# Kernel tuning notes

Measured on AMD Instinct MI355X. Metric: run time of the kernel, lower is better.

## Reference

```python
import jax, jax.numpy as jnp
import numpy as np

BLANK = 0  # blank_index


def lstm_step(x, h, c, W_ih, W_hh, b_ih, b_hh):
    # torch LSTM gate order: i, f, g, o
    gates = x @ W_ih.T + h @ W_hh.T + b_ih + b_hh  # (B, 4H)
    i, f, g, o = jnp.split(gates, 4, axis=-1)
    c2 = jax.nn.sigmoid(f) * c + jax.nn.sigmoid(i) * jnp.tanh(g)
    h2 = jax.nn.sigmoid(o) * jnp.tanh(c2)
    return h2, c2


def greedy_decode(encoder_output, encoded_lengths, embedding, W_ih, W_hh, b_ih, b_hh,
                  W_enc, b_enc, W_pred, b_pred, W_out, b_out, h0, c0):
    # encoder_output: (B, H, T) -> (B, T, H), as in forward()'s transpose(1, 2)
    x = jnp.transpose(encoder_output, (0, 2, 1))
    B, T, H = x.shape

    def step(carry, inputs):
        h, c, last_label = carry          # h,c: (1,B,H); last_label: (B,) int32
        f_t, t = inputs                   # f_t: (B,H) encoder frame, t: scalar int32
        # _pred_step: SOS (zero vector) at t==0, else embed last emitted label
        emb = jnp.where(t == 0, jnp.zeros((B, H), x.dtype), embedding[last_label])
        h1, c1 = lstm_step(emb, h[0], c[0], W_ih, W_hh, b_ih, b_hh)
        # _joint_step: additive joint + relu + output proj, log_softmax (CPU path)
        joint = jax.nn.relu(f_t @ W_enc.T + b_enc + h1 @ W_pred.T + b_pred)
        logp = jax.nn.log_softmax((joint @ W_out.T + b_out).astype(jnp.float32), axis=-1)
        k = jnp.argmax(logp, axis=-1).astype(jnp.int32)  # (B,)
        # blank if past this utterance's length OR argmax is blank
        blank_mask = (t >= encoded_lengths) | (k == BLANK)
        m = blank_mask[:, None]
        # blank entries keep old RNN state and old last_label (original's gather/scatter)
        h_new = jnp.where(m, h[0], h1)[None]
        c_new = jnp.where(m, c[0], c1)[None]
        new_label = jnp.where(blank_mask, last_label, k)
        emitted = jnp.where(blank_mask, BLANK, k)  # blank == nothing emitted this step
        return (h_new, c_new, new_label), emitted

    init = (h0, c0, jnp.full((B,), BLANK, jnp.int32))
    xs = (jnp.transpose(x, (1, 0, 2)), jnp.arange(T, dtype=jnp.int32))
    (hF, cF, _), emitted = jax.lax.scan(step, init, xs)  # emitted: (T, B)
    return emitted.T, hF, cF  # labels (B,T) blank-padded, final (h, c)


def setup_inputs() -> dict:
    key = jax.random.key(0)
    ks = jax.random.split(key, 15)
    B, T, H, V1 = 128, 512, 640, 4097
    s = jnp.float32(0.1)
    return {
        "encoder_output": jax.random.normal(ks[0], (B, H, T), jnp.float32),
        "encoded_lengths": jax.random.randint(ks[1], (B,), 0, T).astype(jnp.int32),
        "embedding": jax.random.normal(ks[2], (V1, H), jnp.float32) * s,
        "W_ih": jax.random.normal(ks[3], (4 * H, H), jnp.float32) * s,
        "W_hh": jax.random.normal(ks[4], (4 * H, H), jnp.float32) * s,
        "b_ih": jax.random.normal(ks[5], (4 * H,), jnp.float32) * s,
        "b_hh": jax.random.normal(ks[6], (4 * H,), jnp.float32) * s,
        "W_enc": jax.random.normal(ks[7], (H, H), jnp.float32) * s,
        "b_enc": jax.random.normal(ks[8], (H,), jnp.float32) * s,
        "W_pred": jax.random.normal(ks[9], (H, H), jnp.float32) * s,
        "b_pred": jax.random.normal(ks[10], (H,), jnp.float32) * s,
        "W_out": jax.random.normal(ks[11], (V1, H), jnp.float32) * s,
        "b_out": jax.random.normal(ks[12], (V1,), jnp.float32) * s,
        "h0": jnp.zeros((1, B, H), jnp.float32),
        "c0": jnp.zeros((1, B, H), jnp.float32),
    }


def reference(encoder_output, encoded_lengths, embedding, W_ih, W_hh, b_ih, b_hh,
              W_enc, b_enc, W_pred, b_pred, W_out, b_out, h0, c0):
    return greedy_decode(encoder_output, encoded_lengths, embedding, W_ih, W_hh,
                         b_ih, b_hh, W_enc, b_enc, W_pred, b_pred, W_out, b_out, h0, c0)
```

## Files before the change

kernel.cpp:

```cpp
#include <hip/hip_runtime.h>
#include <stdint.h>

#define HH 640
#define BB 128
#define TT 512
#define VV 4097
#define G4 2560
#define VP3 4104
#define VE  4112

typedef float f32x4v __attribute__((ext_vector_type(4)));

__device__ __forceinline__ float sigm(float x){ return 1.0f/(1.0f+expf(-x)); }

__device__ __forceinline__ unsigned long long packkey(float f, unsigned v){
    unsigned u = __float_as_uint(f);
    unsigned m = (u & 0x80000000u) ? ~u : (u | 0x80000000u);
    return ((unsigned long long)m << 32) | (unsigned long long)(~v);
}
__device__ __forceinline__ int xcd_tile(int bid, int per){ return (bid & 7)*per + (bid >> 3); }
__device__ __forceinline__ size_t taddr(int k, int b){
    return ((size_t)(k>>2)*BB + b)*4 + (k&3);
}

__global__ __launch_bounds__(256) void k_init3(const float* __restrict__ h0, const float* __restrict__ c0,
                       float* __restrict__ hs0, float* __restrict__ csT,
                       int* __restrict__ label, unsigned long long* __restrict__ slot8){
    int i = blockIdx.x*256 + threadIdx.x;
    if (i < BB*HH){
        int b = i / HH, jj = i % HH;
        size_t o = taddr(jj, b);
        hs0[o] = h0[i]; csT[o] = c0[i];
    }
    if (i < BB) label[i] = 0;
    if (i < 8*BB) slot8[i] = 0ULL;
}

__global__ __launch_bounds__(256) void k_tr_gate(const float* __restrict__ W, float* __restrict__ WT){
    int idx = blockIdx.x*256 + threadIdx.x;
    if (idx >= G4*160) return;
    int row = idx / 160, kq = idx % 160;
    int g = row / HH, jj = row % HH;
    float4 f = *reinterpret_cast<const float4*>(W + (size_t)row*HH + kq*4);
    WT[(size_t)(kq*4+0)*G4 + jj*4+g] = f.x;
    WT[(size_t)(kq*4+1)*G4 + jj*4+g] = f.y;
    WT[(size_t)(kq*4+2)*G4 + jj*4+g] = f.z;
    WT[(size_t)(kq*4+3)*G4 + jj*4+g] = f.w;
}
__global__ __launch_bounds__(256) void k_tr640(const float* __restrict__ W, float* __restrict__ WT){
    int idx = blockIdx.x*256 + threadIdx.x;
    if (idx >= HH*160) return;
    int n = idx / 160, kq = idx % 160;
    float4 f = *reinterpret_cast<const float4*>(W + (size_t)n*HH + kq*4);
    WT[(size_t)(kq*4+0)*HH + n] = f.x;
    WT[(size_t)(kq*4+1)*HH + n] = f.y;
    WT[(size_t)(kq*4+2)*HH + n] = f.z;
    WT[(size_t)(kq*4+3)*HH + n] = f.w;
}
__global__ __launch_bounds__(256) void k_tr_wout3(const float* __restrict__ W, float* __restrict__ WT){
    int idx = blockIdx.x*256 + threadIdx.x;
    if (idx >= VP3*160) return;
    int v = idx / 160, kq = idx % 160;
    float4 f = make_float4(0.f,0.f,0.f,0.f);
    if (v < VV) f = *reinterpret_cast<const float4*>(W + (size_t)v*HH + kq*4);
    WT[(size_t)(kq*4+0)*VP3 + v] = f.x;
    WT[(size_t)(kq*4+1)*VP3 + v] = f.y;
    WT[(size_t)(kq*4+2)*VP3 + v] = f.z;
    WT[(size_t)(kq*4+3)*VP3 + v] = f.w;
}
__global__ __launch_bounds__(256) void k_boutpad3(const float* __restrict__ b_out, float* __restrict__ boutP){
    int v = blockIdx.x*256 + threadIdx.x;
    if (v < VP3) boutP[v] = (v < VV) ? b_out[v] : -1e30f;
}
__global__ __launch_bounds__(256) void k_tr_embT(const float* __restrict__ emb, float* __restrict__ embT){
    int idx = blockIdx.x*256 + threadIdx.x;
    if (idx >= 160*VE) return;
    int kq = idx / VE, v = idx % VE;
    float4 f = make_float4(0.f,0.f,0.f,0.f);
    if (v < VV) f = *reinterpret_cast<const float4*>(emb + (size_t)v*HH + kq*4);
    embT[(size_t)(kq*4+0)*VE + v] = f.x;
    embT[(size_t)(kq*4+1)*VE + v] = f.y;
    embT[(size_t)(kq*4+2)*VE + v] = f.z;
    embT[(size_t)(kq*4+3)*VE + v] = f.w;
}

__global__ __launch_bounds__(256) void k_embproj3(const float* __restrict__ embT,
                          const float* __restrict__ WihT,
                          const float* __restrict__ b_ih, const float* __restrict__ b_hh,
                          float* __restrict__ embproj){
    __shared__ float lwv[HH*16];
    int vt = blockIdx.x / 160, ut = blockIdx.x % 160;
    for (int i=threadIdx.x; i<HH*16; i+=256)
        lwv[i] = WihT[(size_t)(i>>4)*G4 + ut*16 + (i&15)];
    float bias[16];
    #pragma unroll
    for (int u=0;u<16;++u){
        int gu = ut*16+u, jj = gu>>2, g = gu&3;
        bias[u] = b_ih[g*HH+jj] + b_hh[g*HH+jj];
    }
    __syncthreads();
    int v = vt*256 + threadIdx.x;
    float acc[16];
    #pragma unroll
    for (int u=0;u<16;++u) acc[u]=0.f;
    if (v < VV){
        #pragma unroll 2
        for (int k=0;k<HH;++k){
            float e = embT[(size_t)k*VE + v];
            const f32x4v* wr = reinterpret_cast<const f32x4v*>(&lwv[k*16]);
            #pragma unroll
            for (int g=0; g<4; ++g){
                f32x4v w = wr[g];
                #pragma unroll
                for (int ee=0; ee<4; ++ee) acc[g*4+ee] = fmaf(w[ee], e, acc[g*4+ee]);
            }
        }
    }
    if (v <= VV){
        #pragma unroll
        for (int q=0;q<4;++q){
            float4 st = make_float4(acc[q*4+0]+bias[q*4+0], acc[q*4+1]+bias[q*4+1],
                                    acc[q*4+2]+bias[q*4+2], acc[q*4+3]+bias[q*4+3]);
            *reinterpret_cast<float4*>(embproj + (size_t)v*G4 + ut*16 + q*4) = st;
        }
    }
}

__global__ __launch_bounds__(128) void k_encprojT2(const float* __restrict__ x,
                          const float* __restrict__ WencT, const float* __restrict__ b_enc,
                          float* __restrict__ encprojT){
    int tile = (blockIdx.x & 7)*2560 + (blockIdx.x >> 3);
    int b   = tile / 160;
    int rem = tile % 160;
    int tt  = rem / 5;
    int nt2 = rem % 5;
    int n = nt2*128 + threadIdx.x;
    float acc[16];
    #pragma unroll
    for (int i=0;i<16;i++) acc[i]=0.f;
    const float* xb = x + (size_t)b*HH*TT + tt*16;
    #pragma unroll 4
    for (int k=0;k<HH;++k){
        float wv = WencT[(size_t)k*HH + n];
        const float4* xp = reinterpret_cast<const float4*>(xb + (size_t)k*TT);
        float4 x0=xp[0], x1=xp[1], x2=xp[2], x3=xp[3];
        acc[0]=fmaf(x0.x,wv,acc[0]);  acc[1]=fmaf(x0.y,wv,acc[1]);
        acc[2]=fmaf(x0.z,wv,acc[2]);  acc[3]=fmaf(x0.w,wv,acc[3]);
        acc[4]=fmaf(x1.x,wv,acc[4]);  acc[5]=fmaf(x1.y,wv,acc[5]);
        acc[6]=fmaf(x1.z,wv,acc[6]);  acc[7]=fmaf(x1.w,wv,acc[7]);
        acc[8]=fmaf(x2.x,wv,acc[8]);  acc[9]=fmaf(x2.y,wv,acc[9]);
        acc[10]=fmaf(x2.z,wv,acc[10]); acc[11]=fmaf(x2.w,wv,acc[11]);
        acc[12]=fmaf(x3.x,wv,acc[12]); acc[13]=fmaf(x3.y,wv,acc[13]);
        acc[14]=fmaf(x3.z,wv,acc[14]); acc[15]=fmaf(x3.w,wv,acc[15]);
    }
    float be = b_enc[n];
    #pragma unroll
    for (int ti=0; ti<16; ++ti)
        encprojT[((size_t)(tt*16+ti)*HH + n)*BB + b] = acc[ti] + be;
}


__global__ __launch_bounds__(512) void kA(
    const float* __restrict__ WhhT, const float* __restrict__ embproj,
    const int* __restrict__ lens,
    const float* __restrict__ hsrT, float* __restrict__ hswT,
    const float* __restrict__ h1rT, float* __restrict__ h1wT,
    float* __restrict__ csT, float* __restrict__ c1T,
    int* __restrict__ label, const unsigned long long* __restrict__ slot8,
    float* __restrict__ out_emit, int t)
{
    __shared__ float lw[HH*16];
    __shared__ float red[3*16*128];
    const int bid = xcd_tile(blockIdx.x, 20);
    const int tid = threadIdx.x;
    const int b = tid & 127, kh = tid >> 7;
    const int u0 = bid*16;

    for (int i=tid; i<HH*16; i+=512)
        lw[i] = WhhT[(size_t)(i>>4)*G4 + u0 + (i&15)];

    bool mask; int sel=0, kprev=0;
    if (t==0){ mask=true; sel=0; }
    else{
        unsigned long long key = slot8[b];
        #pragma unroll
        for (int q=1;q<8;++q){ unsigned long long o=slot8[q*128+b]; if(o>key)key=o; }
        int k = (int)(~(unsigned)key);
        int lab = label[b];
        mask = ((t-1) >= lens[b]) || (k==0);
        kprev = k; sel = mask ? lab : k;
    }
    __syncthreads();

    const float4* hp = reinterpret_cast<const float4*>(mask ? hsrT : h1rT);
    float a1[16];
    #pragma unroll
    for (int u=0;u<16;++u) a1[u]=0.f;
    const int k0 = kh*40;
    #pragma unroll 2
    for (int k4=k0; k4<k0+40; ++k4){
        float4 hv = hp[(size_t)k4*BB + b];
        #pragma unroll
        for (int q=0;q<4;++q){
            float h = (q==0)?hv.x:(q==1)?hv.y:(q==2)?hv.z:hv.w;
            const f32x4v* wr = reinterpret_cast<const f32x4v*>(&lw[(k4*4+q)*16]);
            #pragma unroll
            for (int g=0; g<4; ++g){
                f32x4v w = wr[g];
                #pragma unroll
                for (int ee=0; ee<4; ++ee) a1[g*4+ee] = fmaf(w[ee], h, a1[g*4+ee]);
            }
        }
    }
    if (kh > 0){
        #pragma unroll
        for (int u=0;u<16;++u) red[((kh-1)*16+u)*128 + b] = a1[u];
    }
    __syncthreads();
    if (kh == 0){
        int erow = (t==0) ? VV : sel;
        const float4* eb = reinterpret_cast<const float4*>(embproj + (size_t)erow*G4 + u0);
        const size_t g4 = (size_t)bid*BB + b;
        float4 ce4 = mask ? reinterpret_cast<const float4*>(csT)[g4]
                          : reinterpret_cast<const float4*>(c1T)[g4];
        float4 he4 = mask ? reinterpret_cast<const float4*>(hsrT)[g4]
                          : reinterpret_cast<const float4*>(h1rT)[g4];
        float cn[4], hn[4];
        const float* cep = &ce4.x;
        #pragma unroll
        for (int jl=0; jl<4; ++jl){
            float4 e = eb[jl];
            float gi = a1[jl*4+0] + red[(jl*4+0)*128+b] + red[(16+jl*4+0)*128+b] + red[(32+jl*4+0)*128+b] + e.x;
            float gf = a1[jl*4+1] + red[(jl*4+1)*128+b] + red[(16+jl*4+1)*128+b] + red[(32+jl*4+1)*128+b] + e.y;
            float gg = a1[jl*4+2] + red[(jl*4+2)*128+b] + red[(16+jl*4+2)*128+b] + red[(32+jl*4+2)*128+b] + e.z;
            float go = a1[jl*4+3] + red[(jl*4+3)*128+b] + red[(16+jl*4+3)*128+b] + red[(32+jl*4+3)*128+b] + e.w;
            float ce = cep[jl];
            float cv = sigm(gf)*ce + sigm(gi)*tanhf(gg);
            cn[jl] = cv;
            hn[jl] = sigm(go)*tanhf(cv);
        }
        reinterpret_cast<float4*>(csT)[g4]  = ce4;
        reinterpret_cast<float4*>(c1T)[g4]  = make_float4(cn[0],cn[1],cn[2],cn[3]);
        reinterpret_cast<float4*>(hswT)[g4] = he4;
        reinterpret_cast<float4*>(h1wT)[g4] = make_float4(hn[0],hn[1],hn[2],hn[3]);
        if (bid == 0){
            if (t > 0) out_emit[(size_t)b*TT + (t-1)] = mask ? 0.f : (float)kprev;
            label[b] = sel;
        }
    }
}

__global__ __launch_bounds__(512) void kB(
    const float* __restrict__ WpredT, const float* __restrict__ encprojT,
    const float* __restrict__ b_pred, const float* __restrict__ h1T,
    float* __restrict__ jointT, unsigned long long* __restrict__ slot8, int t)
{
    __shared__ float lw[HH*4];
    __shared__ float red[3*4*128];
    const int bid = xcd_tile(blockIdx.x, 20);
    const int tid = threadIdx.x;
    const int b = tid & 127, kh = tid >> 7;
    const int n0 = bid*4;
    for (int i=tid; i<HH*4; i+=512)
        lw[i] = WpredT[(size_t)(i>>2)*HH + n0 + (i&3)];
    if (bid == 0 && kh == 3){
        #pragma unroll
        for (int q=0;q<8;++q) slot8[q*128 + b] = 0ULL;
    }
    __syncthreads();
    const float4* hp = reinterpret_cast<const float4*>(h1T);
    float a[4] = {0.f,0.f,0.f,0.f};
    const int k0 = kh*40;
    #pragma unroll 2
    for (int k4=k0; k4<k0+40; ++k4){
        float4 hv = hp[(size_t)k4*BB + b];
        #pragma unroll
        for (int q=0;q<4;++q){
            float h = (q==0)?hv.x:(q==1)?hv.y:(q==2)?hv.z:hv.w;
            f32x4v w = *reinterpret_cast<const f32x4v*>(&lw[(k4*4+q)*4]);
            #pragma unroll
            for (int ee=0; ee<4; ++ee) a[ee] = fmaf(w[ee], h, a[ee]);
        }
    }
    if (kh > 0){
        #pragma unroll
        for (int u=0;u<4;++u) red[((kh-1)*4+u)*128 + b] = a[u];
    }
    __syncthreads();
    if (kh == 0){
        float jn[4];
        #pragma unroll
        for (int u=0;u<4;++u){
            float s = a[u] + red[u*128+b] + red[(4+u)*128+b] + red[(8+u)*128+b]
                    + b_pred[n0+u] + encprojT[((size_t)t*HH + n0+u)*BB + b];
            jn[u] = fmaxf(s, 0.f);
        }
        reinterpret_cast<float4*>(jointT)[(size_t)bid*BB + b] =
            make_float4(jn[0],jn[1],jn[2],jn[3]);
    }
}

__global__ __launch_bounds__(512) void kC(
    const float* __restrict__ WoutT3, const float* __restrict__ boutP3,
    const float* __restrict__ jointT, unsigned long long* __restrict__ slot8)
{
    __shared__ float lw[HH*20];
    __shared__ float red[3*19*128];
    const int bid = xcd_tile(blockIdx.x, 27);
    const int tid = threadIdx.x;
    const int b = tid & 127, kh = tid >> 7;
    const int v0 = bid*19;
    for (int i=tid; i<HH*19; i+=512){
        int k = i/19, u = i - k*19;
        lw[k*20 + u] = WoutT3[(size_t)k*VP3 + v0 + u];
    }
    __syncthreads();
    const float4* jp = reinterpret_cast<const float4*>(jointT);
    float a[19];
    #pragma unroll
    for (int u=0;u<19;++u) a[u]=0.f;
    const int k0 = kh*40;
    #pragma unroll 2
    for (int k4=k0; k4<k0+40; ++k4){
        float4 jv = jp[(size_t)k4*BB + b];
        #pragma unroll
        for (int q=0;q<4;++q){
            float h = (q==0)?jv.x:(q==1)?jv.y:(q==2)?jv.z:jv.w;
            const f32x4v* wr = reinterpret_cast<const f32x4v*>(&lw[(k4*4+q)*20]);
            #pragma unroll
            for (int g=0; g<4; ++g){
                f32x4v w = wr[g];
                #pragma unroll
                for (int ee=0; ee<4; ++ee) a[g*4+ee] = fmaf(w[ee], h, a[g*4+ee]);
            }
            f32x4v w4 = wr[4];
            a[16] = fmaf(w4[0], h, a[16]);
            a[17] = fmaf(w4[1], h, a[17]);
            a[18] = fmaf(w4[2], h, a[18]);
        }
    }
    if (kh > 0){
        #pragma unroll
        for (int u=0;u<19;++u) red[((kh-1)*19+u)*128 + b] = a[u];
    }
    __syncthreads();
    if (kh == 0){
        unsigned long long key = 0ULL;
        #pragma unroll
        for (int u=0;u<19;++u){
            float s = a[u] + red[u*128+b] + red[(19+u)*128+b] + red[(38+u)*128+b] + boutP3[v0+u];
            unsigned long long kk = packkey(s, (unsigned)(v0+u));
            if (kk > key) key = kk;
        }
        atomicMax(&slot8[(bid&7)*128 + b], key);
    }
}

__global__ __launch_bounds__(256) void kFin(const int* __restrict__ lens,
                        const unsigned long long* __restrict__ slot8,
                        const float* __restrict__ hsT, const float* __restrict__ h1T,
                        const float* __restrict__ csT, const float* __restrict__ c1T,
                        float* __restrict__ dout)
{
    int i = blockIdx.x*256 + threadIdx.x;
    if (i >= BB*HH) return;
    int b = i / HH, jj = i % HH;
    unsigned long long key = slot8[b];
    #pragma unroll
    for (int q=1;q<8;++q){ unsigned long long o=slot8[q*128+b]; if(o>key)key=o; }
    int k = (int)(~(unsigned)key);
    bool m = ((TT-1) >= lens[b]) || (k == 0);
    size_t o = taddr(jj, b);
    dout[BB*TT + i]         = m ? hsT[o] : h1T[o];
    dout[BB*TT + BB*HH + i] = m ? csT[o] : c1T[o];
    if (i < BB){
        unsigned long long key2 = slot8[i];
        #pragma unroll
        for (int q=1;q<8;++q){ unsigned long long o2=slot8[q*128+i]; if(o2>key2)key2=o2; }
        int k2 = (int)(~(unsigned)key2);
        bool mm = ((TT-1) >= lens[i]) || (k2 == 0);
        dout[(size_t)i*TT + (TT-1)] = mm ? 0.0f : (float)k2;
    }
}

__global__ __launch_bounds__(256) void k_init(const float* __restrict__ h0, const float* __restrict__ c0,
                       float* __restrict__ hs0, float* __restrict__ cs,
                       int* __restrict__ label, unsigned long long* __restrict__ slot){
    int i = blockIdx.x*256 + threadIdx.x;
    if (i < BB*HH){ hs0[i] = h0[i]; cs[i] = c0[i]; }
    if (i < BB){ label[i] = 0; slot[i] = 0ULL; }
}

__global__ __launch_bounds__(256) void k_p1o(
    const float* __restrict__ Whh, const float* __restrict__ Wih,
    const float* __restrict__ embedding,
    const float* __restrict__ b_ih, const float* __restrict__ b_hh,
    const int* __restrict__ lens,
    const float* __restrict__ hs_r, float* __restrict__ hs_w,
    const float* __restrict__ h1_r, float* __restrict__ h1_w,
    float* c_state, float* c1, int* label,
    const unsigned long long* __restrict__ slot,
    float* __restrict__ out_emit, int t)
{
    int tile = (blockIdx.x & 7)*20 + (blockIdx.x >> 3);
    int jt = tile >> 4, bg = tile & 15;
    int lane = threadIdx.x & 63, w = threadIdx.x >> 6;
    int j = (jt<<6) + lane, b0 = bg<<3;

    bool mask[8]; int kprev[8]; int sel[8];
    #pragma unroll
    for (int bi=0; bi<8; ++bi){
        int b = b0+bi;
        if (t == 0){ mask[bi]=true; sel[bi]=0; kprev[bi]=0; }
        else {
            unsigned long long key = slot[b];
            int k = (int)(~(unsigned)key);
            int lab = label[b];
            bool m = ((t-1) >= lens[b]) || (k == 0);
            mask[bi]=m; kprev[bi]=k; sel[bi] = m ? lab : k;
        }
    }
    float acc[8];
    #pragma unroll
    for (int i=0;i<8;i++) acc[i]=0.f;
    const float* wrow  = Whh + (size_t)(w*HH + j)*HH;
    const float* wrow2 = Wih + (size_t)(w*HH + j)*HH;
    for (int kc=0; kc<HH; kc+=16){
        float wv[16], wv2[16];
        #pragma unroll
        for (int q=0;q<4;q++){
            float4 f = *reinterpret_cast<const float4*>(wrow + kc + q*4);
            wv[q*4+0]=f.x; wv[q*4+1]=f.y; wv[q*4+2]=f.z; wv[q*4+3]=f.w;
            float4 f2 = *reinterpret_cast<const float4*>(wrow2 + kc + q*4);
            wv2[q*4+0]=f2.x; wv2[q*4+1]=f2.y; wv2[q*4+2]=f2.z; wv2[q*4+3]=f2.w;
        }
        #pragma unroll
        for (int bi=0; bi<8; ++bi){
            int b = b0+bi;
            const float* hp0 = hs_r + (size_t)b*HH + kc;
            const float* hp1 = h1_r + (size_t)b*HH + kc;
            float a = acc[bi];
            if (mask[bi]){
                #pragma unroll
                for (int k=0;k<16;k++) a = fmaf(hp0[k], wv[k], a);
            } else {
                #pragma unroll
                for (int k=0;k<16;k++) a = fmaf(hp1[k], wv[k], a);
            }
            if (t > 0){
                const float* ep = embedding + (size_t)sel[bi]*HH + kc;
                #pragma unroll
                for (int k=0;k<16;k++) a = fmaf(ep[k], wv2[k], a);
            }
            acc[bi] = a;
        }
    }
    __shared__ float xch[8][4][64];
    #pragma unroll
    for (int bi=0; bi<8; ++bi)
        xch[bi][w][lane] = acc[bi] + b_ih[w*HH + j] + b_hh[w*HH + j];
    __syncthreads();
    #pragma unroll
    for (int r=0; r<2; ++r){
        int bi = (w<<1) + r;
        int b  = b0 + bi;
        size_t o = (size_t)b*HH + j;
        float gi = xch[bi][0][lane], gf = xch[bi][1][lane];
        float gg = xch[bi][2][lane], go = xch[bi][3][lane];
        float ce = mask[bi] ? c_state[o] : c1[o];
        float c2 = sigm(gf)*ce + sigm(gi)*tanhf(gg);
        float h2 = sigm(go)*tanhf(c2);
        float he = mask[bi] ? hs_r[o] : h1_r[o];
        c_state[o] = ce; c1[o] = c2; hs_w[o] = he; h1_w[o] = h2;
    }
    if (jt == 0 && t > 0 && threadIdx.x < 8){
        int bi = threadIdx.x; int b = b0 + bi;
        out_emit[(size_t)b*TT + (t-1)] = mask[bi] ? 0.0f : (float)kprev[bi];
        label[b] = sel[bi];
    }
}

__global__ __launch_bounds__(128) void k_p2o(
    const float* __restrict__ Wpred, const float* __restrict__ Wenc,
    const float* __restrict__ x, const float* __restrict__ b_enc,
    const float* __restrict__ b_pred, const float* __restrict__ h1,
    float* __restrict__ joint, unsigned long long* __restrict__ slot, int t)
{
    int tile = (blockIdx.x & 7)*20 + (blockIdx.x >> 3);
    int nt = tile / 32, bg = tile % 32;
    int lane = threadIdx.x & 63, w = threadIdx.x >> 6;
    int n = nt*128 + w*64 + lane, b0 = bg*4;
    float acc[4] = {0.f,0.f,0.f,0.f};
    const float* wr  = Wpred + (size_t)n*HH;
    const float* wr2 = Wenc  + (size_t)n*HH;
    for (int kc=0; kc<HH; kc+=16){
        float wv[16], wv2[16];
        #pragma unroll
        for (int q=0;q<4;q++){
            float4 f = *reinterpret_cast<const float4*>(wr + kc + q*4);
            wv[q*4+0]=f.x; wv[q*4+1]=f.y; wv[q*4+2]=f.z; wv[q*4+3]=f.w;
            float4 f2 = *reinterpret_cast<const float4*>(wr2 + kc + q*4);
            wv2[q*4+0]=f2.x; wv2[q*4+1]=f2.y; wv2[q*4+2]=f2.z; wv2[q*4+3]=f2.w;
        }
        #pragma unroll
        for (int bi=0; bi<4; ++bi){
            int b = b0+bi;
            const float* hp = h1 + (size_t)b*HH + kc;
            float a = acc[bi];
            #pragma unroll
            for (int k=0;k<16;k++) a = fmaf(hp[k], wv[k], a);
            const float* xp = x + (size_t)b*HH*TT + (size_t)kc*TT + t;
            #pragma unroll
            for (int k=0;k<16;k++) a = fmaf(xp[(size_t)k*TT], wv2[k], a);
            acc[bi] = a;
        }
    }
    #pragma unroll
    for (int bi=0; bi<4; ++bi){
        int b = b0+bi;
        joint[(size_t)b*HH + n] = fmaxf(acc[bi] + b_pred[n] + b_enc[n], 0.0f);
    }
    if (tile == 0) slot[threadIdx.x] = 0ULL;
}

__global__ __launch_bounds__(256) void k_p3o(
    const float* __restrict__ Wout, const float* __restrict__ b_out,
    const float* __restrict__ joint, unsigned long long* __restrict__ slot)
{
    int tile = (blockIdx.x & 7)*34 + (blockIdx.x >> 3);
    int vt = tile >> 4, bg = tile & 15;
    int lane = threadIdx.x & 63, w = threadIdx.x >> 6;
    int v = vt*256 + w*64 + lane;
    bool valid = v < VV;
    int vv = valid ? v : (VV-1);
    int b0 = bg*8;
    float acc[8];
    #pragma unroll
    for (int i=0;i<8;i++) acc[i]=0.f;
    const float* wr = Wout + (size_t)vv*HH;
    for (int kc=0; kc<HH; kc+=16){
        float wv[16];
        #pragma unroll
        for (int q=0;q<4;q++){
            float4 f = *reinterpret_cast<const float4*>(wr + kc + q*4);
            wv[q*4+0]=f.x; wv[q*4+1]=f.y; wv[q*4+2]=f.z; wv[q*4+3]=f.w;
        }
        #pragma unroll
        for (int bi=0; bi<8; ++bi){
            int b = b0+bi;
            const float* jp = joint + (size_t)b*HH + kc;
            float a = acc[bi];
            #pragma unroll
            for (int k=0;k<16;k++) a = fmaf(jp[k], wv[k], a);
            acc[bi] = a;
        }
    }
    float bofl = b_out[vv];
    __shared__ unsigned long long redo[4][8];
    #pragma unroll
    for (int bi=0; bi<8; ++bi){
        unsigned long long key = valid ? packkey(acc[bi] + bofl, (unsigned)v) : 0ULL;
        #pragma unroll
        for (int off=32; off>0; off>>=1){
            unsigned long long o = __shfl_xor(key, off, 64);
            if (o > key) key = o;
        }
        if (lane == 0) redo[w][bi] = key;
    }
    __syncthreads();
    if (threadIdx.x < 8){
        int bi = threadIdx.x;
        unsigned long long m = redo[0][bi];
        #pragma unroll
        for (int q=1;q<4;q++) if (redo[q][bi] > m) m = redo[q][bi];
        atomicMax(&slot[b0+bi], m);
    }
}

__global__ __launch_bounds__(256) void k_finalo(const int* __restrict__ lens,
                        const unsigned long long* __restrict__ slot,
                        const float* __restrict__ hs_r, const float* __restrict__ h1_r,
                        const float* __restrict__ cs,  const float* __restrict__ c1,
                        float* __restrict__ dout)
{
    int i = blockIdx.x*256 + threadIdx.x;
    if (i >= BB*HH) return;
    int b = i / HH;
    unsigned long long key = slot[b];
    int k = (int)(~(unsigned)key);
    bool m = ((TT-1) >= lens[b]) || (k == 0);
    dout[BB*TT + i]         = m ? hs_r[i] : h1_r[i];
    dout[BB*TT + BB*HH + i] = m ? cs[i]   : c1[i];
    if (i < BB){
        unsigned long long key2 = slot[i];
        int k2 = (int)(~(unsigned)key2);
        bool mm = ((TT-1) >= lens[i]) || (k2 == 0);
        dout[(size_t)i*TT + (TT-1)] = mm ? 0.0f : (float)k2;
    }
}

extern "C" void kernel_launch(void* const* d_in, const int* in_sizes, int n_in,
                              void* d_out, int out_size, void* d_ws, size_t ws_size,
                              hipStream_t stream)
{
    const float* x     = (const float*)d_in[0];
    const int*   lens  = (const int*)  d_in[1];
    const float* emb   = (const float*)d_in[2];
    const float* Wih   = (const float*)d_in[3];
    const float* Whh   = (const float*)d_in[4];
    const float* bih   = (const float*)d_in[5];
    const float* bhh   = (const float*)d_in[6];
    const float* Wenc  = (const float*)d_in[7];
    const float* benc  = (const float*)d_in[8];
    const float* Wpred = (const float*)d_in[9];
    const float* bpred = (const float*)d_in[10];
    const float* Wout  = (const float*)d_in[11];
    const float* bout  = (const float*)d_in[12];
    const float* h0    = (const float*)d_in[13];
    const float* c0    = (const float*)d_in[14];
    float* out = (float*)d_out;
    (void)in_sizes; (void)n_in; (void)out_size;

    char* ws = (char*)d_ws;
    size_t off = 0;
    auto alloc = [&](size_t bytes) -> void* {
        void* p = ws + off; off += (bytes + 255) & ~(size_t)255; return p;
    };
    auto aligned = [](size_t bytes){ return (bytes + 255) & ~(size_t)255; };

    const size_t BH = (size_t)BB*HH*sizeof(float);
    float* hs0  = (float*)alloc(BH);
    float* hs1  = (float*)alloc(BH);
    float* h1b0 = (float*)alloc(BH);
    float* h1b1 = (float*)alloc(BH);
    float* cs   = (float*)alloc(BH);
    float* c1   = (float*)alloc(BH);
    float* joint= (float*)alloc(BH);
    int* label  = (int*)alloc(BB*sizeof(int));
    unsigned long long* slot8 = (unsigned long long*)alloc(8*BB*sizeof(unsigned long long));

    size_t need = off
        + aligned((size_t)HH*G4*sizeof(float))
        + aligned((size_t)HH*G4*sizeof(float))
        + aligned((size_t)HH*HH*sizeof(float))
        + aligned((size_t)HH*HH*sizeof(float))
        + aligned((size_t)HH*VP3*sizeof(float))
        + aligned((size_t)VP3*sizeof(float))
        + aligned((size_t)HH*VE*sizeof(float))
        + aligned((size_t)(VV+1)*G4*sizeof(float))
        + aligned((size_t)TT*BB*HH*sizeof(float));

    if (ws_size >= need){
        float* WhhT   = (float*)alloc((size_t)HH*G4*sizeof(float));
        float* WihT   = (float*)alloc((size_t)HH*G4*sizeof(float));
        float* WpredT = (float*)alloc((size_t)HH*HH*sizeof(float));
        float* WencT  = (float*)alloc((size_t)HH*HH*sizeof(float));
        float* WoutT3 = (float*)alloc((size_t)HH*VP3*sizeof(float));
        float* boutP3 = (float*)alloc((size_t)VP3*sizeof(float));
        float* embT   = (float*)alloc((size_t)HH*VE*sizeof(float));
        float* embproj= (float*)alloc((size_t)(VV+1)*G4*sizeof(float));
        float* encprojT=(float*)alloc((size_t)TT*BB*HH*sizeof(float));

        k_init3<<<(BB*HH+255)/256, 256, 0, stream>>>(h0, c0, hs0, cs, label, slot8);
        k_tr_gate<<<(G4*160+255)/256, 256, 0, stream>>>(Whh, WhhT);
        k_tr_gate<<<(G4*160+255)/256, 256, 0, stream>>>(Wih, WihT);
        k_tr640 <<<(HH*160+255)/256, 256, 0, stream>>>(Wpred, WpredT);
        k_tr640 <<<(HH*160+255)/256, 256, 0, stream>>>(Wenc,  WencT);
        k_tr_wout3<<<(VP3*160+255)/256, 256, 0, stream>>>(Wout, WoutT3);
        k_boutpad3<<<(VP3+255)/256, 256, 0, stream>>>(bout, boutP3);
        k_tr_embT<<<(160*VE+255)/256, 256, 0, stream>>>(emb, embT);
        k_embproj3<<<17*160, 256, 0, stream>>>(embT, WihT, bih, bhh, embproj);
        k_encprojT2<<<20480, 128, 0, stream>>>(x, WencT, benc, encprojT);

        float* hsbuf[2] = {hs0, hs1};
        float* h1buf[2] = {h1b0, h1b1};
        for (int t = 0; t < TT; ++t){
            const float* hsr = hsbuf[t & 1];
            float*       hsw = hsbuf[(t+1) & 1];
            const float* h1r = h1buf[(t+1) & 1];
            float*       h1w = h1buf[t & 1];
            kA<<<160, 512, 0, stream>>>(WhhT, embproj, lens, hsr, hsw, h1r, h1w,
                                        cs, c1, label, slot8, out, t);
            kB<<<160, 512, 0, stream>>>(WpredT, encprojT, bpred, h1w, joint, slot8, t);
            kC<<<216, 512, 0, stream>>>(WoutT3, boutP3, joint, slot8);
        }
        kFin<<<(BB*HH+255)/256, 256, 0, stream>>>(lens, slot8, hsbuf[0], h1buf[1], cs, c1, out);
        return;
    }

    unsigned long long* slot = slot8;
    k_init<<<(BB*HH+255)/256, 256, 0, stream>>>(h0, c0, hs0, cs, label, slot);
    float* hsbuf[2] = {hs0, hs1};
    float* h1buf[2] = {h1b0, h1b1};
    for (int t = 0; t < TT; ++t){
        const float* hsr = hsbuf[t & 1];
        float*       hsw = hsbuf[(t+1) & 1];
        const float* h1r = h1buf[(t+1) & 1];
        float*       h1w = h1buf[t & 1];
        k_p1o<<<160, 256, 0, stream>>>(Whh, Wih, emb, bih, bhh, lens,
                                       hsr, hsw, h1r, h1w, cs, c1, label, slot, out, t);
        k_p2o<<<160, 128, 0, stream>>>(Wpred, Wenc, x, benc, bpred, h1w, joint, slot, t);
        k_p3o<<<272, 256, 0, stream>>>(Wout, bout, joint, slot);
    }
    k_finalo<<<(BB*HH+255)/256, 256, 0, stream>>>(lens, slot, hsbuf[0], h1buf[1], cs, c1, out);
}
```

Measured before the change: 33.09 ms.

## Pre-pack per-block weight tiles contiguously and rebalance output projection to 16-wide tiles

```diff
diff --git a/kernel.cpp b/kernel.cpp
--- a/kernel.cpp
+++ b/kernel.cpp
@@ -6,8 +6,7 @@
 #define TT 512
 #define VV 4097
 #define G4 2560
-#define VP3 4104
-#define VE  4112
+#define VP3 4352
 
 typedef float f32x4v __attribute__((ext_vector_type(4)));
 
@@ -57,7 +56,7 @@
     WT[(size_t)(kq*4+2)*HH + n] = f.z;
     WT[(size_t)(kq*4+3)*HH + n] = f.w;
 }
-__global__ __launch_bounds__(256) void k_tr_wout3(const float* __restrict__ W, float* __restrict__ WT){
+__global__ __launch_bounds__(256) void k_tr_woutr(const float* __restrict__ W, float* __restrict__ WT){
     int idx = blockIdx.x*256 + threadIdx.x;
     if (idx >= VP3*160) return;
     int v = idx / 160, kq = idx % 160;
@@ -68,30 +67,43 @@
     WT[(size_t)(kq*4+2)*VP3 + v] = f.z;
     WT[(size_t)(kq*4+3)*VP3 + v] = f.w;
 }
-__global__ __launch_bounds__(256) void k_boutpad3(const float* __restrict__ b_out, float* __restrict__ boutP){
+__global__ __launch_bounds__(256) void k_boutp(const float* __restrict__ b_out, float* __restrict__ bp){
     int v = blockIdx.x*256 + threadIdx.x;
-    if (v < VP3) boutP[v] = (v < VV) ? b_out[v] : -1e30f;
-}
-__global__ __launch_bounds__(256) void k_tr_embT(const float* __restrict__ emb, float* __restrict__ embT){
-    int idx = blockIdx.x*256 + threadIdx.x;
-    if (idx >= 160*VE) return;
-    int kq = idx / VE, v = idx % VE;
-    float4 f = make_float4(0.f,0.f,0.f,0.f);
-    if (v < VV) f = *reinterpret_cast<const float4*>(emb + (size_t)v*HH + kq*4);
-    embT[(size_t)(kq*4+0)*VE + v] = f.x;
-    embT[(size_t)(kq*4+1)*VE + v] = f.y;
-    embT[(size_t)(kq*4+2)*VE + v] = f.z;
-    embT[(size_t)(kq*4+3)*VE + v] = f.w;
-}
-
-__global__ __launch_bounds__(256) void k_embproj3(const float* __restrict__ embT,
+    if (v < VP3) bp[v] = (v < VV) ? b_out[v] : -1e30f;
+}
+
+__global__ __launch_bounds__(256) void k_packA(const float* __restrict__ WhhT, float* __restrict__ WhhP){
+    int i = blockIdx.x*256 + threadIdx.x;
+    if (i >= 160*HH*4) return;
+    int bid = i / (HH*4), rem = i % (HH*4);
+    int k = rem >> 2, q = rem & 3;
+    reinterpret_cast<float4*>(WhhP)[i] =
+        *reinterpret_cast<const float4*>(&WhhT[(size_t)k*G4 + bid*16 + q*4]);
+}
+__global__ __launch_bounds__(256) void k_packB(const float* __restrict__ WpredT, float* __restrict__ WpredP){
+    int i = blockIdx.x*256 + threadIdx.x;
+    if (i >= 160*HH) return;
+    int bid = i / HH, k = i % HH;
+    reinterpret_cast<float4*>(WpredP)[i] =
+        *reinterpret_cast<const float4*>(&WpredT[(size_t)k*HH + bid*4]);
+}
+__global__ __launch_bounds__(256) void k_packC(const float* __restrict__ WoutTr, float* __restrict__ WoutP){
+    int i = blockIdx.x*256 + threadIdx.x;
+    if (i >= 272*HH*4) return;
+    int bid = i / (HH*4), rem = i % (HH*4);
+    int k = rem >> 2, q = rem & 3;
+    reinterpret_cast<float4*>(WoutP)[i] =
+        *reinterpret_cast<const float4*>(&WoutTr[(size_t)k*VP3 + bid*16 + q*4]);
+}
+
+__global__ __launch_bounds__(256) void k_embproj2(const float* __restrict__ emb,
                           const float* __restrict__ WihT,
                           const float* __restrict__ b_ih, const float* __restrict__ b_hh,
                           float* __restrict__ embproj){
-    __shared__ float lwv[HH*16];
+    __shared__ float lw[640*16];
     int vt = blockIdx.x / 160, ut = blockIdx.x % 160;
-    for (int i=threadIdx.x; i<HH*16; i+=256)
-        lwv[i] = WihT[(size_t)(i>>4)*G4 + ut*16 + (i&15)];
+    for (int i=threadIdx.x; i<640*16; i+=256)
+        lw[i] = WihT[(size_t)(i>>4)*G4 + ut*16 + (i&15)];
     float bias[16];
     #pragma unroll
     for (int u=0;u<16;++u){
@@ -104,15 +116,19 @@
     #pragma unroll
     for (int u=0;u<16;++u) acc[u]=0.f;
     if (v < VV){
-        #pragma unroll 2
-        for (int k=0;k<HH;++k){
-            float e = embT[(size_t)k*VE + v];
-            const f32x4v* wr = reinterpret_cast<const f32x4v*>(&lwv[k*16]);
+        const float4* er = reinterpret_cast<const float4*>(emb + (size_t)v*HH);
+        for (int k4=0;k4<160;++k4){
+            float4 ev = er[k4];
             #pragma unroll
-            for (int g=0; g<4; ++g){
-                f32x4v w = wr[g];
+            for (int q=0;q<4;++q){
+                float e = (q==0)?ev.x:(q==1)?ev.y:(q==2)?ev.z:ev.w;
+                const f32x4v* wr = reinterpret_cast<const f32x4v*>(&lw[(k4*4+q)*16]);
                 #pragma unroll
-                for (int ee=0; ee<4; ++ee) acc[g*4+ee] = fmaf(w[ee], e, acc[g*4+ee]);
+                for (int g=0; g<4; ++g){
+                    f32x4v w = wr[g];
+                    #pragma unroll
+                    for (int ee=0; ee<4; ++ee) acc[g*4+ee] = fmaf(w[ee], e, acc[g*4+ee]);
+                }
             }
         }
     }
@@ -161,7 +177,7 @@
 
 
 __global__ __launch_bounds__(512) void kA(
-    const float* __restrict__ WhhT, const float* __restrict__ embproj,
+    const float* __restrict__ WhhP, const float* __restrict__ embproj,
     const int* __restrict__ lens,
     const float* __restrict__ hsrT, float* __restrict__ hswT,
     const float* __restrict__ h1rT, float* __restrict__ h1wT,
@@ -176,8 +192,11 @@
     const int b = tid & 127, kh = tid >> 7;
     const int u0 = bid*16;
 
-    for (int i=tid; i<HH*16; i+=512)
-        lw[i] = WhhT[(size_t)(i>>4)*G4 + u0 + (i&15)];
+    {
+        const float4* wsrc = reinterpret_cast<const float4*>(WhhP + (size_t)bid*(HH*16));
+        float4* ld = reinterpret_cast<float4*>(lw);
+        for (int i=tid; i<HH*4; i+=512) ld[i] = wsrc[i];
+    }
 
     bool mask; int sel=0, kprev=0;
     if (t==0){ mask=true; sel=0; }
@@ -197,7 +216,7 @@
     #pragma unroll
     for (int u=0;u<16;++u) a1[u]=0.f;
     const int k0 = kh*40;
-    #pragma unroll 2
+    #pragma unroll 4
     for (int k4=k0; k4<k0+40; ++k4){
         float4 hv = hp[(size_t)k4*BB + b];
         #pragma unroll
@@ -251,7 +270,7 @@
 }
 
 __global__ __launch_bounds__(512) void kB(
-    const float* __restrict__ WpredT, const float* __restrict__ encprojT,
+    const float* __restrict__ WpredP, const float* __restrict__ encprojT,
     const float* __restrict__ b_pred, const float* __restrict__ h1T,
     float* __restrict__ jointT, unsigned long long* __restrict__ slot8, int t)
 {
@@ -261,8 +280,11 @@
     const int tid = threadIdx.x;
     const int b = tid & 127, kh = tid >> 7;
     const int n0 = bid*4;
-    for (int i=tid; i<HH*4; i+=512)
-        lw[i] = WpredT[(size_t)(i>>2)*HH + n0 + (i&3)];
+    {
+        const float4* wsrc = reinterpret_cast<const float4*>(WpredP + (size_t)bid*(HH*4));
+        float4* ld = reinterpret_cast<float4*>(lw);
+        for (int i=tid; i<HH; i+=512) ld[i] = wsrc[i];
+    }
     if (bid == 0 && kh == 3){
         #pragma unroll
         for (int q=0;q<8;++q) slot8[q*128 + b] = 0ULL;
@@ -271,7 +293,7 @@
     const float4* hp = reinterpret_cast<const float4*>(h1T);
     float a[4] = {0.f,0.f,0.f,0.f};
     const int k0 = kh*40;
-    #pragma unroll 2
+    #pragma unroll 4
     for (int k4=k0; k4<k0+40; ++k4){
         float4 hv = hp[(size_t)k4*BB + b];
         #pragma unroll
@@ -301,54 +323,51 @@
 }
 
 __global__ __launch_bounds__(512) void kC(
-    const float* __restrict__ WoutT3, const float* __restrict__ boutP3,
+    const float* __restrict__ WoutP, const float* __restrict__ boutP,
     const float* __restrict__ jointT, unsigned long long* __restrict__ slot8)
 {
-    __shared__ float lw[HH*20];
-    __shared__ float red[3*19*128];
-    const int bid = xcd_tile(blockIdx.x, 27);
+    __shared__ float lw[HH*16];
+    __shared__ float red[3*16*128];
+    const int bid = xcd_tile(blockIdx.x, 34);
     const int tid = threadIdx.x;
     const int b = tid & 127, kh = tid >> 7;
-    const int v0 = bid*19;
-    for (int i=tid; i<HH*19; i+=512){
-        int k = i/19, u = i - k*19;
-        lw[k*20 + u] = WoutT3[(size_t)k*VP3 + v0 + u];
+    const int v0 = bid*16;
+    {
+        const float4* wsrc = reinterpret_cast<const float4*>(WoutP + (size_t)bid*(HH*16));
+        float4* ld = reinterpret_cast<float4*>(lw);
+        for (int i=tid; i<HH*4; i+=512) ld[i] = wsrc[i];
     }
     __syncthreads();
     const float4* jp = reinterpret_cast<const float4*>(jointT);
-    float a[19];
-    #pragma unroll
-    for (int u=0;u<19;++u) a[u]=0.f;
+    float a[16];
+    #pragma unroll
+    for (int u=0;u<16;++u) a[u]=0.f;
     const int k0 = kh*40;
-    #pragma unroll 2
+    #pragma unroll 4
     for (int k4=k0; k4<k0+40; ++k4){
         float4 jv = jp[(size_t)k4*BB + b];
         #pragma unroll
         for (int q=0;q<4;++q){
             float h = (q==0)?jv.x:(q==1)?jv.y:(q==2)?jv.z:jv.w;
-            const f32x4v* wr = reinterpret_cast<const f32x4v*>(&lw[(k4*4+q)*20]);
+            const f32x4v* wr = reinterpret_cast<const f32x4v*>(&lw[(k4*4+q)*16]);
             #pragma unroll
             for (int g=0; g<4; ++g){
                 f32x4v w = wr[g];
                 #pragma unroll
                 for (int ee=0; ee<4; ++ee) a[g*4+ee] = fmaf(w[ee], h, a[g*4+ee]);
             }
-            f32x4v w4 = wr[4];
-            a[16] = fmaf(w4[0], h, a[16]);
-            a[17] = fmaf(w4[1], h, a[17]);
-            a[18] = fmaf(w4[2], h, a[18]);
         }
     }
     if (kh > 0){
         #pragma unroll
-        for (int u=0;u<19;++u) red[((kh-1)*19+u)*128 + b] = a[u];
+        for (int u=0;u<16;++u) red[((kh-1)*16+u)*128 + b] = a[u];
     }
     __syncthreads();
     if (kh == 0){
         unsigned long long key = 0ULL;
         #pragma unroll
-        for (int u=0;u<19;++u){
-            float s = a[u] + red[u*128+b] + red[(19+u)*128+b] + red[(38+u)*128+b] + boutP3[v0+u];
+        for (int u=0;u<16;++u){
+            float s = a[u] + red[u*128+b] + red[(16+u)*128+b] + red[(32+u)*128+b] + boutP[v0+u];
             unsigned long long kk = packkey(s, (unsigned)(v0+u));
             if (kk > key) key = kk;
         }
@@ -384,10 +403,10 @@
 }
 
 __global__ __launch_bounds__(256) void k_init(const float* __restrict__ h0, const float* __restrict__ c0,
-                       float* __restrict__ hs0, float* __restrict__ cs,
+                       float* __restrict__ hs0, float* __restrict__ cso,
                        int* __restrict__ label, unsigned long long* __restrict__ slot){
     int i = blockIdx.x*256 + threadIdx.x;
-    if (i < BB*HH){ hs0[i] = h0[i]; cs[i] = c0[i]; }
+    if (i < BB*HH){ hs0[i] = h0[i]; cso[i] = c0[i]; }
     if (i < BB){ label[i] = 0; slot[i] = 0ULL; }
 }
 
@@ -398,7 +417,7 @@
     const int* __restrict__ lens,
     const float* __restrict__ hs_r, float* __restrict__ hs_w,
     const float* __restrict__ h1_r, float* __restrict__ h1_w,
-    float* c_state, float* c1, int* label,
+    float* c_state, float* c1o, int* label,
     const unsigned long long* __restrict__ slot,
     float* __restrict__ out_emit, int t)
 {
@@ -461,17 +480,17 @@
         xch[bi][w][lane] = acc[bi] + b_ih[w*HH + j] + b_hh[w*HH + j];
     __syncthreads();
     #pragma unroll
-    for (int r=0; r<2; ++r){
-        int bi = (w<<1) + r;
+    for (int rr=0; rr<2; ++rr){
+        int bi = (w<<1) + rr;
         int b  = b0 + bi;
         size_t o = (size_t)b*HH + j;
         float gi = xch[bi][0][lane], gf = xch[bi][1][lane];
         float gg = xch[bi][2][lane], go = xch[bi][3][lane];
-        float ce = mask[bi] ? c_state[o] : c1[o];
+        float ce = mask[bi] ? c_state[o] : c1o[o];
         float c2 = sigm(gf)*ce + sigm(gi)*tanhf(gg);
         float h2 = sigm(go)*tanhf(c2);
         float he = mask[bi] ? hs_r[o] : h1_r[o];
-        c_state[o] = ce; c1[o] = c2; hs_w[o] = he; h1_w[o] = h2;
+        c_state[o] = ce; c1o[o] = c2; hs_w[o] = he; h1_w[o] = h2;
     }
     if (jt == 0 && t > 0 && threadIdx.x < 8){
         int bi = threadIdx.x; int b = b0 + bi;
@@ -580,7 +599,7 @@
 __global__ __launch_bounds__(256) void k_finalo(const int* __restrict__ lens,
                         const unsigned long long* __restrict__ slot,
                         const float* __restrict__ hs_r, const float* __restrict__ h1_r,
-                        const float* __restrict__ cs,  const float* __restrict__ c1,
+                        const float* __restrict__ cso,  const float* __restrict__ c1o,
                         float* __restrict__ dout)
 {
     int i = blockIdx.x*256 + threadIdx.x;
@@ -590,7 +609,7 @@
     int k = (int)(~(unsigned)key);
     bool m = ((TT-1) >= lens[b]) || (k == 0);
     dout[BB*TT + i]         = m ? hs_r[i] : h1_r[i];
-    dout[BB*TT + BB*HH + i] = m ? cs[i]   : c1[i];
+    dout[BB*TT + BB*HH + i] = m ? cso[i]  : c1o[i];
     if (i < BB){
         unsigned long long key2 = slot[i];
         int k2 = (int)(~(unsigned)key2);
@@ -626,8 +645,6 @@
     auto alloc = [&](size_t bytes) -> void* {
         void* p = ws + off; off += (bytes + 255) & ~(size_t)255; return p;
     };
-    auto aligned = [](size_t bytes){ return (bytes + 255) & ~(size_t)255; };
-
     const size_t BH = (size_t)BB*HH*sizeof(float);
     float* hs0  = (float*)alloc(BH);
     float* hs1  = (float*)alloc(BH);
@@ -638,38 +655,33 @@
     float* joint= (float*)alloc(BH);
     int* label  = (int*)alloc(BB*sizeof(int));
     unsigned long long* slot8 = (unsigned long long*)alloc(8*BB*sizeof(unsigned long long));
-
-    size_t need = off
-        + aligned((size_t)HH*G4*sizeof(float))
-        + aligned((size_t)HH*G4*sizeof(float))
-        + aligned((size_t)HH*HH*sizeof(float))
-        + aligned((size_t)HH*HH*sizeof(float))
-        + aligned((size_t)HH*VP3*sizeof(float))
-        + aligned((size_t)VP3*sizeof(float))
-        + aligned((size_t)HH*VE*sizeof(float))
-        + aligned((size_t)(VV+1)*G4*sizeof(float))
-        + aligned((size_t)TT*BB*HH*sizeof(float));
+    float* boutP = (float*)alloc((size_t)VP3*sizeof(float));
+    float* WencT = (float*)alloc((size_t)HH*HH*sizeof(float));
+    float* WhhP  = (float*)alloc((size_t)160*HH*16*sizeof(float));
+    float* WpredP= (float*)alloc((size_t)160*HH*4*sizeof(float));
+    float* WoutP = (float*)alloc((size_t)272*HH*16*sizeof(float));
+    float* embproj  = (float*)alloc((size_t)(VV+1)*G4*sizeof(float));
+    float* encprojT = (float*)alloc((size_t)TT*BB*HH*sizeof(float));
+    size_t need = off;
 
     if (ws_size >= need){
-        float* WhhT   = (float*)alloc((size_t)HH*G4*sizeof(float));
-        float* WihT   = (float*)alloc((size_t)HH*G4*sizeof(float));
-        float* WpredT = (float*)alloc((size_t)HH*HH*sizeof(float));
-        float* WencT  = (float*)alloc((size_t)HH*HH*sizeof(float));
-        float* WoutT3 = (float*)alloc((size_t)HH*VP3*sizeof(float));
-        float* boutP3 = (float*)alloc((size_t)VP3*sizeof(float));
-        float* embT   = (float*)alloc((size_t)HH*VE*sizeof(float));
-        float* embproj= (float*)alloc((size_t)(VV+1)*G4*sizeof(float));
-        float* encprojT=(float*)alloc((size_t)TT*BB*HH*sizeof(float));
+        char* A = (char*)encprojT;
+        float* WhhT   = (float*)(A);
+        float* WoutTr = (float*)(A + 7340032);
+        float* WihT   = (float*)(A + 19922944);
+        float* WpredT = (float*)(A + 27262976);
 
         k_init3<<<(BB*HH+255)/256, 256, 0, stream>>>(h0, c0, hs0, cs, label, slot8);
         k_tr_gate<<<(G4*160+255)/256, 256, 0, stream>>>(Whh, WhhT);
+        k_packA<<<(160*HH*4+255)/256, 256, 0, stream>>>(WhhT, WhhP);
+        k_tr640<<<(HH*160+255)/256, 256, 0, stream>>>(Wpred, WpredT);
+        k_packB<<<(160*HH+255)/256, 256, 0, stream>>>(WpredT, WpredP);
+        k_tr_woutr<<<(VP3*160+255)/256, 256, 0, stream>>>(Wout, WoutTr);
+        k_packC<<<(272*HH*4+255)/256, 256, 0, stream>>>(WoutTr, WoutP);
+        k_boutp<<<(VP3+255)/256, 256, 0, stream>>>(bout, boutP);
         k_tr_gate<<<(G4*160+255)/256, 256, 0, stream>>>(Wih, WihT);
-        k_tr640 <<<(HH*160+255)/256, 256, 0, stream>>>(Wpred, WpredT);
-        k_tr640 <<<(HH*160+255)/256, 256, 0, stream>>>(Wenc,  WencT);
-        k_tr_wout3<<<(VP3*160+255)/256, 256, 0, stream>>>(Wout, WoutT3);
-        k_boutpad3<<<(VP3+255)/256, 256, 0, stream>>>(bout, boutP3);
-        k_tr_embT<<<(160*VE+255)/256, 256, 0, stream>>>(emb, embT);
-        k_embproj3<<<17*160, 256, 0, stream>>>(embT, WihT, bih, bhh, embproj);
+        k_embproj2<<<17*160, 256, 0, stream>>>(emb, WihT, bih, bhh, embproj);
+        k_tr640<<<(HH*160+255)/256, 256, 0, stream>>>(Wenc, WencT);
         k_encprojT2<<<20480, 128, 0, stream>>>(x, WencT, benc, encprojT);
 
         float* hsbuf[2] = {hs0, hs1};
@@ -679,28 +691,43 @@
             float*       hsw = hsbuf[(t+1) & 1];
             const float* h1r = h1buf[(t+1) & 1];
             float*       h1w = h1buf[t & 1];
-            kA<<<160, 512, 0, stream>>>(WhhT, embproj, lens, hsr, hsw, h1r, h1w,
+            kA<<<160, 512, 0, stream>>>(WhhP, embproj, lens, hsr, hsw, h1r, h1w,
                                         cs, c1, label, slot8, out, t);
-            kB<<<160, 512, 0, stream>>>(WpredT, encprojT, bpred, h1w, joint, slot8, t);
-            kC<<<216, 512, 0, stream>>>(WoutT3, boutP3, joint, slot8);
+            kB<<<160, 512, 0, stream>>>(WpredP, encprojT, bpred, h1w, joint, slot8, t);
+            kC<<<272, 512, 0, stream>>>(WoutP, boutP, joint, slot8);
         }
         kFin<<<(BB*HH+255)/256, 256, 0, stream>>>(lens, slot8, hsbuf[0], h1buf[1], cs, c1, out);
         return;
     }
 
-    unsigned long long* slot = slot8;
-    k_init<<<(BB*HH+255)/256, 256, 0, stream>>>(h0, c0, hs0, cs, label, slot);
-    float* hsbuf[2] = {hs0, hs1};
-    float* h1buf[2] = {h1b0, h1b1};
-    for (int t = 0; t < TT; ++t){
-        const float* hsr = hsbuf[t & 1];
-        float*       hsw = hsbuf[(t+1) & 1];
-        const float* h1r = h1buf[(t+1) & 1];
-        float*       h1w = h1buf[t & 1];
-        k_p1o<<<160, 256, 0, stream>>>(Whh, Wih, emb, bih, bhh, lens,
-                                       hsr, hsw, h1r, h1w, cs, c1, label, slot, out, t);
-        k_p2o<<<160, 128, 0, stream>>>(Wpred, Wenc, x, benc, bpred, h1w, joint, slot, t);
-        k_p3o<<<272, 256, 0, stream>>>(Wout, bout, joint, slot);
-    }
-    k_finalo<<<(BB*HH+255)/256, 256, 0, stream>>>(lens, slot, hsbuf[0], h1buf[1], cs, c1, out);
-}
+    {
+        size_t foff = 0;
+        auto falloc = [&](size_t bytes) -> void* {
+            void* p = ws + foff; foff += (bytes + 255) & ~(size_t)255; return p;
+        };
+        float* fhs0  = (float*)falloc(BH);
+        float* fhs1  = (float*)falloc(BH);
+        float* fh1b0 = (float*)falloc(BH);
+        float* fh1b1 = (float*)falloc(BH);
+        float* fcs   = (float*)falloc(BH);
+        float* fc1   = (float*)falloc(BH);
+        float* fjoint= (float*)falloc(BH);
+        int* flabel  = (int*)falloc(BB*sizeof(int));
+        unsigned long long* fslot = (unsigned long long*)falloc(BB*sizeof(unsigned long long));
+
+        k_init<<<(BB*HH+255)/256, 256, 0, stream>>>(h0, c0, fhs0, fcs, flabel, fslot);
+        float* hsbuf[2] = {fhs0, fhs1};
+        float* h1buf[2] = {fh1b0, fh1b1};
+        for (int t = 0; t < TT; ++t){
+            const float* hsr = hsbuf[t & 1];
+            float*       hsw = hsbuf[(t+1) & 1];
+            const float* h1r = h1buf[(t+1) & 1];
+            float*       h1w = h1buf[t & 1];
+            k_p1o<<<160, 256, 0, stream>>>(Whh, Wih, emb, bih, bhh, lens,
+                                           hsr, hsw, h1r, h1w, fcs, fc1, flabel, fslot, out, t);
+            k_p2o<<<160, 128, 0, stream>>>(Wpred, Wenc, x, benc, bpred, h1w, fjoint, fslot, t);
+            k_p3o<<<272, 256, 0, stream>>>(Wout, bout, fjoint, fslot);
+        }
+        k_finalo<<<(BB*HH+255)/256, 256, 0, stream>>>(lens, fslot, hsbuf[0], h1buf[1], fcs, fc1, out);
+    }
+}
```

Result: faster. 30.09 ms (-9.1%).
